# Kernel tuning notes

Hardware: AMD Instinct MI355X
Metric: run time of the kernel (lower is better)

Reference implementation:

```python
import jax, jax.numpy as jnp
import numpy as np


def setup_inputs() -> dict:
    key = jax.random.key(0)
    k1, k2, k3 = jax.random.split(key, 3)
    B, C, N, K, O = 8, 64, 4096, 16, 64
    x = jax.random.normal(k1, (B, C, N, 1), dtype=jnp.float32)
    # 1x1 Conv2d weights (out, in*2), biases (out)
    W_edge = jax.random.normal(k2, (O, 2 * C), dtype=jnp.float32) * 0.05
    b_edge = jnp.zeros((O,), dtype=jnp.float32)
    W_att = jax.random.normal(k3, (O, 2 * C), dtype=jnp.float32) * 0.05
    b_att = jnp.zeros((O,), dtype=jnp.float32)
    return {"x": x, "W_edge": W_edge, "b_edge": b_edge,
            "W_att": W_att, "b_att": b_att, "k": K}


def reference(x, W_edge, b_edge, W_att, b_att, k):
    # x: (B, C, N, 1)
    xt = jnp.transpose(x[..., 0], (0, 2, 1))  # (B, N, C)

    # --- dense KNN via pairwise squared distance (no-grad in original) ---
    xd = jax.lax.stop_gradient(xt)
    sq = jnp.sum(xd * xd, axis=-1, keepdims=True)           # (B, N, 1)
    dist = sq - 2.0 * jnp.einsum('bnc,bmc->bnm', xd, xd) + jnp.transpose(sq, (0, 2, 1))
    _, nn_idx = jax.lax.top_k(-dist, k)                      # (B, N, k)

    # --- gather neighbor features ---
    x_j = jax.vmap(lambda feat, idx: feat[idx])(xt, nn_idx)  # (B, N, k, C)
    # center index gather is identity: x_i[b,n,kk] = xt[b,n]
    x_i = jnp.broadcast_to(xt[:, :, None, :], x_j.shape)     # (B, N, k, C)

    feat = jnp.concatenate([x_i, x_j - x_i], axis=-1)        # (B, N, k, 2C)

    # 1x1 convs == per-point linear over channels
    edge = jnp.einsum('bnkc,oc->bnko', feat, W_edge) + b_edge  # (B, N, k, O)
    attn = jnp.einsum('bnkc,oc->bnko', feat, W_att) + b_att
    attn = jax.nn.softmax(attn, axis=2)                        # softmax over k

    out = jnp.sum(edge * attn, axis=2)                         # (B, N, O)
    # match torch output layout (B, O, N, 1)
    return jnp.transpose(out, (0, 2, 1))[..., None]
```

## Files before the change

### kernel.cpp

```cpp
#include <hip/hip_runtime.h>
#include <hip/hip_bf16.h>
#include <stdint.h>

#define NB 8
#define NC 64
#define NN 4096
#define NK 16
#define NO 64
#define TILE 64
#define NCHUNK 2
#define CHCOLS (NN / NCHUNK)
#define NTILES (CHCOLS / TILE)
#define NKL 16
#define NKC 32
#define PQS 160

typedef __attribute__((ext_vector_type(8))) short bf16x8;
typedef __attribute__((ext_vector_type(4))) float f32x4;

__device__ __forceinline__ unsigned umin32(unsigned a, unsigned b) { return a < b ? a : b; }
__device__ __forceinline__ unsigned shflx(unsigned v, int m) {
  return (unsigned)__shfl_xor((int)v, m);
}
__device__ __forceinline__ unsigned fmap(float x) {
  unsigned u = __float_as_uint(x);
  return u ^ ((unsigned)((int)u >> 31) | 0x80000000u);
}

__device__ __forceinline__ void cvt16bf(const float4 st[4], uint4& lo, uint4& hi) {
  union { float4 v[4]; float f[16]; } in;
  in.v[0] = st[0]; in.v[1] = st[1]; in.v[2] = st[2]; in.v[3] = st[3];
  union { unsigned short h[16]; uint4 v[2]; } out;
  #pragma unroll
  for (int i = 0; i < 16; ++i) {
    __hip_bfloat16 hh = __float2bfloat16(in.f[i]);
    out.h[i] = *reinterpret_cast<unsigned short*>(&hh);
  }
  lo = out.v[0]; hi = out.v[1];
}

__global__ __launch_bounds__(256) void proj_kernel(
    const float* __restrict__ x, const float* __restrict__ We,
    const float* __restrict__ be, const float* __restrict__ Wa,
    float* __restrict__ PQ, float* __restrict__ sq,
    float* __restrict__ XT)
{
  __shared__ float xs[NC][TILE];
  __shared__ float wt[NC][192];
  const int bid = blockIdx.x;
  const int b   = bid >> 6;
  const int n0  = (bid & 63) * TILE;
  const int tid = threadIdx.x;

  const float4* xg4 = (const float4*)x;
  float4* xs4 = (float4*)xs;
  for (int i = tid; i < NC * TILE / 4; i += 256) {
    int c = i >> 4, p4 = i & 15;
    xs4[c * 16 + p4] = xg4[(b * NC + c) * (NN / 4) + (n0 >> 2) + p4];
  }
  for (int i = tid; i < 64 * NC; i += 256) {
    int o = i >> 6, c = i & 63;
    float w1 = We[o * 128 + c], w2 = We[o * 128 + 64 + c];
    wt[c][o]        = w1 - w2;
    wt[c][64 + o]   = w2;
    wt[c][128 + o]  = Wa[o * 128 + 64 + c];
  }
  __syncthreads();

  {
    const int p = tid & 63, cg = tid >> 6;
    float4 v4[4];
    #pragma unroll
    for (int g = 0; g < 4; ++g) {
      v4[g].x = xs[cg * 16 + g * 4 + 0][p];
      v4[g].y = xs[cg * 16 + g * 4 + 1][p];
      v4[g].z = xs[cg * 16 + g * 4 + 2][p];
      v4[g].w = xs[cg * 16 + g * 4 + 3][p];
    }
    float4* Xp = (float4*)(XT + ((size_t)(b * NN + n0 + p) * NC + cg * 16));
    Xp[0] = v4[0]; Xp[1] = v4[1]; Xp[2] = v4[2]; Xp[3] = v4[3];
  }

  if (tid >= 192) {
    int p = tid - 192;
    float s = 0.f;
    #pragma unroll
    for (int c = 0; c < NC; ++c) { float v = xs[c][p]; s = fmaf(v, v, s); }
    sq[b * NN + n0 + p] = s;
  } else {
    const int r = tid;
    float wreg[NC];
    #pragma unroll
    for (int c = 0; c < NC; ++c) wreg[c] = wt[c][r];
    const float bias = (r < 64) ? be[r] : 0.f;
    for (int p = 0; p < TILE; p += 4) {
      float a0 = bias, a1 = bias, a2 = bias, a3 = bias;
      #pragma unroll
      for (int c = 0; c < NC; ++c) {
        float4 xv = *(const float4*)&xs[c][p];
        a0 = fmaf(wreg[c], xv.x, a0);
        a1 = fmaf(wreg[c], xv.y, a1);
        a2 = fmaf(wreg[c], xv.z, a2);
        a3 = fmaf(wreg[c], xv.w, a3);
      }
      if (r < 128) {
        size_t base = (size_t)(b * NN + n0 + p) * PQS + r;
        PQ[base]           = a0;
        PQ[base + PQS]     = a1;
        PQ[base + 2 * PQS] = a2;
        PQ[base + 3 * PQS] = a3;
      } else {
        const int o = r - 128;
        unsigned short* qb = (unsigned short*)((char*)PQ + (size_t)(b * NN + n0 + p) * (PQS * 4) + 512) + o;
        const size_t stride = PQS * 2;
        __hip_bfloat16 h0 = __float2bfloat16(a0);
        __hip_bfloat16 h1 = __float2bfloat16(a1);
        __hip_bfloat16 h2 = __float2bfloat16(a2);
        __hip_bfloat16 h3 = __float2bfloat16(a3);
        qb[0]          = *reinterpret_cast<unsigned short*>(&h0);
        qb[stride]     = *reinterpret_cast<unsigned short*>(&h1);
        qb[2 * stride] = *reinterpret_cast<unsigned short*>(&h2);
        qb[3 * stride] = *reinterpret_cast<unsigned short*>(&h3);
      }
    }
  }
}

__global__ __launch_bounds__(256) void knn_kernel(
    const float* __restrict__ XT, const float* __restrict__ sq,
    unsigned short* __restrict__ cand)
{
  __shared__ unsigned short Hc[2][64 * 64];
  __shared__ unsigned short Hr[64 * 64];

  const int bid = blockIdx.x;
  const int b   = bid >> 7;
  const int rt  = (bid >> 1) & 63;
  const int ch  = bid & 1;
  const int r0  = rt * TILE;
  const int c0  = ch * CHCOLS;
  const int tid = threadIdx.x;
  const int w    = tid >> 6;
  const int lane = tid & 63;
  const int lm   = lane & 15;
  const int lk   = lane >> 4;

  const float* Xb  = XT + (size_t)b * NN * NC;
  const float* sqg = sq + (size_t)b * NN;

  const int rowS = tid >> 2, subS = tid & 3;
  const int bytS = rowS * 128 + subS * 32;
  const int swzS = (rowS & 7) << 4;

  {
    float4 st[4]; uint4 lo, hi;
    const float4* srcR = (const float4*)(Xb + (size_t)(r0 + rowS) * NC + subS * 16);
    st[0]=srcR[0]; st[1]=srcR[1]; st[2]=srcR[2]; st[3]=srcR[3];
    cvt16bf(st, lo, hi);
    *(uint4*)((char*)Hr + ((bytS)      ^ swzS)) = lo;
    *(uint4*)((char*)Hr + ((bytS + 16) ^ swzS)) = hi;
    const float4* srcC = (const float4*)(Xb + (size_t)(c0 + rowS) * NC + subS * 16);
    st[0]=srcC[0]; st[1]=srcC[1]; st[2]=srcC[2]; st[3]=srcC[3];
    cvt16bf(st, lo, hi);
    *(uint4*)((char*)Hc[0] + ((bytS)      ^ swzS)) = lo;
    *(uint4*)((char*)Hc[0] + ((bytS + 16) ^ swzS)) = hi;
  }
  __syncthreads();

  const int brow = w * 16 + lm;
  const int bswz = (brow & 7) << 4;
  const bf16x8 bf0 = *(const bf16x8*)((const char*)Hr + ((brow * 128 + lk * 16)      ^ bswz));
  const bf16x8 bf1 = *(const bf16x8*)((const char*)Hr + ((brow * 128 + lk * 16 + 64) ^ bswz));

  unsigned bv[NKL];
  #pragma unroll
  for (int t = 0; t < NKL; ++t) bv[t] = 0xFFFFFFFFu;
  unsigned rowGuard = 0xFFFFFFFFu;

  for (int t = 0; t < NTILES; ++t) {
    const int cur = t & 1;
    float4 st[4];
    const bool doStage = (t + 1 < NTILES);
    if (doStage) {
      const float4* src = (const float4*)(Xb + (size_t)(c0 + (t + 1) * TILE + rowS) * NC + subS * 16);
      st[0]=src[0]; st[1]=src[1]; st[2]=src[2]; st[3]=src[3];
    }
    const int n1 = c0 + t * TILE;

    f32x4 acc[4];
    #pragma unroll
    for (int ct = 0; ct < 4; ++ct) acc[ct] = (f32x4){0.f, 0.f, 0.f, 0.f};
    #pragma unroll
    for (int ct = 0; ct < 4; ++ct) {
      const int arow = ct * 16 + lm;
      const int aswz = (arow & 7) << 4;
      bf16x8 a0 = *(const bf16x8*)((const char*)Hc[cur] + ((arow * 128 + lk * 16)      ^ aswz));
      bf16x8 a1 = *(const bf16x8*)((const char*)Hc[cur] + ((arow * 128 + lk * 16 + 64) ^ aswz));
      acc[ct] = __builtin_amdgcn_mfma_f32_16x16x32_bf16(a0, bf0, acc[ct], 0, 0, 0);
      acc[ct] = __builtin_amdgcn_mfma_f32_16x16x32_bf16(a1, bf1, acc[ct], 0, 0, 0);
    }

    unsigned d[16];
    #pragma unroll
    for (int ct = 0; ct < 4; ++ct) {
      const float4 s4 = *(const float4*)&sqg[n1 + ct * 16 + lk * 4];
      const int cbase = (t << 6) + (ct << 4) + (lk << 2);
      d[ct*4+0] = (fmap(fmaf(-2.f, acc[ct][0], s4.x)) & 0xFFFFF800u) | (unsigned)(cbase + 0);
      d[ct*4+1] = (fmap(fmaf(-2.f, acc[ct][1], s4.y)) & 0xFFFFF800u) | (unsigned)(cbase + 1);
      d[ct*4+2] = (fmap(fmaf(-2.f, acc[ct][2], s4.z)) & 0xFFFFF800u) | (unsigned)(cbase + 2);
      d[ct*4+3] = (fmap(fmaf(-2.f, acc[ct][3], s4.w)) & 0xFFFFF800u) | (unsigned)(cbase + 3);
    }

    unsigned m = d[0];
    #pragma unroll
    for (int i = 1; i < 16; ++i) m = umin32(m, d[i]);
    unsigned guard = umin32(bv[NKL - 1], rowGuard);
    #pragma unroll 1
    for (int rnd = 0; rnd < 16; ++rnd) {
      bool ins = m < guard;
      if (!__any(ins)) break;
      unsigned x  = ins ? m : 0xFFFFFFFFu;
      const unsigned xv = x;
      #pragma unroll
      for (int i = 0; i < NKL; ++i) {
        unsigned lo = umin32(bv[i], x);
        x = bv[i] < x ? x : bv[i];
        bv[i] = lo;
      }
      #pragma unroll
      for (int i = 0; i < 16; ++i) d[i] = (d[i] == xv) ? 0xFFFFFFFFu : d[i];
      m = d[0];
      #pragma unroll
      for (int i = 1; i < 16; ++i) m = umin32(m, d[i]);
      unsigned g15 = bv[NKL - 1];
      g15 = umin32(g15, shflx(g15, 16));
      g15 = umin32(g15, shflx(g15, 32));
      rowGuard = g15;
      guard = rowGuard;
    }

    if (doStage) {
      uint4 lo, hi;
      cvt16bf(st, lo, hi);
      *(uint4*)((char*)Hc[cur ^ 1] + ((bytS)      ^ swzS)) = lo;
      *(uint4*)((char*)Hc[cur ^ 1] + ((bytS + 16) ^ swzS)) = hi;
    }
    __syncthreads();
  }

  unsigned* mv = (unsigned*)&Hc[0][0];
  const int myrow = w * 16 + lm;
  __syncthreads();
  #pragma unroll
  for (int t = 0; t < NKL; ++t) mv[(myrow * 4 + lk) * NKL + t] = bv[t];
  __syncthreads();
  if (lk == 0) {
    for (int s2 = 1; s2 < 4; ++s2) {
      for (int t = 0; t < NKL; ++t) {
        unsigned v = mv[(myrow * 4 + s2) * NKL + t];
        if (v >= bv[NKL - 1]) break;
        unsigned x = v;
        #pragma unroll
        for (int q = 0; q < NKL; ++q) {
          unsigned lo = umin32(bv[q], x);
          x = bv[q] < x ? x : bv[q];
          bv[q] = lo;
        }
      }
    }
    unsigned short* cp = cand + (size_t)(b * NN + r0 + myrow) * NKC + ch * NKL;
    #pragma unroll
    for (int t = 0; t < NKL; ++t)
      cp[t] = (unsigned short)((bv[t] & 0x7FFu) + c0);
  }
}

__global__ __launch_bounds__(256) void rescore_kernel(
    const float* __restrict__ XT, const float* __restrict__ sq,
    unsigned short* __restrict__ cand, int* __restrict__ nn_idx)
{
  __shared__ float dv[8][NKC];
  __shared__ unsigned short di[8][NKC];
  const int tid  = threadIdx.x;
  const int w    = tid >> 6;
  const int lane = tid & 63;
  const int rowL = w * 2 + (lane >> 5);
  const int q    = lane & 31;
  const int row  = blockIdx.x * 8 + rowL;
  const int b = row >> 12, n = row & (NN - 1);
  const float* xt  = XT + (size_t)b * NN * NC;
  const float* sqg = sq + (size_t)b * NN;

  const int j = (int)cand[(size_t)row * NKC + q];
  const float4* cj = (const float4*)(xt + (size_t)j * NC);
  const float4* cn = (const float4*)(xt + (size_t)n * NC);
  float s = 0.f;
  #pragma unroll
  for (int i = 0; i < 16; ++i) {
    float4 a = cn[i], bb = cj[i];
    s = fmaf(a.x, bb.x, s);
    s = fmaf(a.y, bb.y, s);
    s = fmaf(a.z, bb.z, s);
    s = fmaf(a.w, bb.w, s);
  }
  dv[rowL][q] = fmaf(-2.f, s, sqg[j]);
  di[rowL][q] = (unsigned short)j;
  __syncthreads();

  if (tid < 8) {
    const int row2 = blockIdx.x * 8 + tid;
    float bvv[NK]; int bbi[NK];
    #pragma unroll
    for (int p = 0; p < NK; ++p) { bvv[p] = 3.0e38f; bbi[p] = 0; }
    for (int t = 0; t < NKC; ++t) {
      float v = dv[tid][t];
      if (v < bvv[NK - 1]) {
        bvv[NK - 1] = v; bbi[NK - 1] = (int)di[tid][t];
        #pragma unroll
        for (int p = NK - 1; p > 0; --p) {
          if (bvv[p] < bvv[p - 1]) {
            float tv = bvv[p]; bvv[p] = bvv[p - 1]; bvv[p - 1] = tv;
            int   ti = bbi[p]; bbi[p] = bbi[p - 1]; bbi[p - 1] = ti;
          }
        }
      }
    }
    int* np = nn_idx + (size_t)row2 * NK;
    #pragma unroll
    for (int p = 0; p < NK; ++p) np[p] = bbi[p];
  }
}

__global__ __launch_bounds__(256) void out_kernel(
    const float* __restrict__ PQ, const int* __restrict__ nn_idx,
    float* __restrict__ out)
{
  __shared__ float ot[TILE][TILE + 1];
  const int bid = blockIdx.x;
  const int b   = bid >> 6;
  const int n0  = (bid & 63) * TILE;
  const int tid = threadIdx.x;
  const int w = tid >> 6, o = tid & 63;

  for (int pi = 0; pi < 16; ++pi) {
    const int p = w * 16 + pi;
    const int n = n0 + p;
    const float* pqn = PQ + (size_t)(b * NN + n) * PQS;
    const float p1b  = pqn[o];
    const int* idxp  = nn_idx + (size_t)(b * NN + n) * NK;
    float p2[NK], q2[NK];
    #pragma unroll
    for (int t = 0; t < NK; ++t) {
      int jn = idxp[t];
      const float* pqj = PQ + (size_t)(b * NN + jn) * PQS;
      p2[t] = pqj[64 + o];
      unsigned short qh = ((const unsigned short*)(pqj + 128))[o];
      q2[t] = __bfloat162float(*reinterpret_cast<__hip_bfloat16*>(&qh));
    }
    float m = q2[0];
    #pragma unroll
    for (int t = 1; t < NK; ++t) m = fmaxf(m, q2[t]);
    float s = 0.f, num = 0.f;
    #pragma unroll
    for (int t = 0; t < NK; ++t) {
      float e = __expf(q2[t] - m);
      s += e;
      num = fmaf(e, p1b + p2[t], num);
    }
    ot[p][o] = num / s;
  }
  __syncthreads();

  const int oo = tid >> 2, qq = tid & 3;
  float* og = out + (size_t)(b * NO + oo) * NN + n0 + qq * 16;
  #pragma unroll
  for (int i = 0; i < 4; ++i) {
    float4 v;
    v.x = ot[qq * 16 + i * 4 + 0][oo];
    v.y = ot[qq * 16 + i * 4 + 1][oo];
    v.z = ot[qq * 16 + i * 4 + 2][oo];
    v.w = ot[qq * 16 + i * 4 + 3][oo];
    *(float4*)&og[i * 4] = v;
  }
}

extern "C" void kernel_launch(void* const* d_in, const int* in_sizes, int n_in,
                              void* d_out, int out_size, void* d_ws, size_t ws_size,
                              hipStream_t stream)
{
  const float* x  = (const float*)d_in[0];
  const float* We = (const float*)d_in[1];
  const float* be = (const float*)d_in[2];
  const float* Wa = (const float*)d_in[3];
  float* out = (float*)d_out;

  char* ws = (char*)d_ws;
  size_t off = 0;
  float* sq = (float*)(ws + off);                  off += (size_t)NB * NN * 4;
  float* PQ = (float*)(ws + off);                  off += (size_t)NB * NN * PQS * 4;
  float* XT = (float*)(ws + off);                  off += (size_t)NB * NN * NC * 4;
  unsigned short* cand = (unsigned short*)(ws + off);
  int* nn = (int*)cand;

  dim3 blk(256);
  proj_kernel<<<dim3(NB * (NN / TILE)), blk, 0, stream>>>(x, We, be, Wa, PQ, sq, XT);
  knn_kernel<<<dim3(NB * (NN / TILE) * NCHUNK), blk, 0, stream>>>(XT, sq, cand);
  rescore_kernel<<<dim3(NB * NN / 8), blk, 0, stream>>>(XT, sq, cand, nn);
  out_kernel<<<dim3(NB * (NN / TILE)), blk, 0, stream>>>(PQ, nn, out);
}
```

Measured before the change: 292.9 us.

## Precompute bf16 features, store projections in bf16, add fast-reject in KNN

The projection kernel now writes a bf16 copy of the transposed features, so the KNN kernel streams half the bytes and no longer converts from fp32 on every tile load. The P1/P2 projection table is stored in bf16 (192 shorts per point) instead of mixed fp32/bf16, which halves the gather traffic in the output kernel. The KNN inner loop first takes a float minimum and skips building packed keys when no lane can beat its current guard. The cost is lower precision in the P projections and an extra bf16 buffer written by proj_kernel.

Result: faster. 284.2 us (-3.0%).

```diff
diff --git a/kernel.cpp b/kernel.cpp
--- a/kernel.cpp
+++ b/kernel.cpp
@@ -13,7 +13,6 @@
 #define NTILES (CHCOLS / TILE)
 #define NKL 16
 #define NKC 32
-#define PQS 160
 
 typedef __attribute__((ext_vector_type(8))) short bf16x8;
 typedef __attribute__((ext_vector_type(4))) float f32x4;
@@ -26,24 +25,19 @@
   unsigned u = __float_as_uint(x);
   return u ^ ((unsigned)((int)u >> 31) | 0x80000000u);
 }
-
-__device__ __forceinline__ void cvt16bf(const float4 st[4], uint4& lo, uint4& hi) {
-  union { float4 v[4]; float f[16]; } in;
-  in.v[0] = st[0]; in.v[1] = st[1]; in.v[2] = st[2]; in.v[3] = st[3];
-  union { unsigned short h[16]; uint4 v[2]; } out;
-  #pragma unroll
-  for (int i = 0; i < 16; ++i) {
-    __hip_bfloat16 hh = __float2bfloat16(in.f[i]);
-    out.h[i] = *reinterpret_cast<unsigned short*>(&hh);
-  }
-  lo = out.v[0]; hi = out.v[1];
+__device__ __forceinline__ float bf2f(unsigned short h) {
+  return __bfloat162float(*reinterpret_cast<__hip_bfloat16*>(&h));
+}
+__device__ __forceinline__ unsigned short f2bfu(float v) {
+  __hip_bfloat16 hh = __float2bfloat16(v);
+  return *reinterpret_cast<unsigned short*>(&hh);
 }
 
 __global__ __launch_bounds__(256) void proj_kernel(
     const float* __restrict__ x, const float* __restrict__ We,
     const float* __restrict__ be, const float* __restrict__ Wa,
-    float* __restrict__ PQ, float* __restrict__ sq,
-    float* __restrict__ XT)
+    unsigned short* __restrict__ PQb, float* __restrict__ sq,
+    float* __restrict__ XT, unsigned short* __restrict__ H)
 {
   __shared__ float xs[NC][TILE];
   __shared__ float wt[NC][192];
@@ -69,16 +63,21 @@
 
   {
     const int p = tid & 63, cg = tid >> 6;
-    float4 v4[4];
+    union { float4 v4[4]; float f[16]; } vv;
     #pragma unroll
     for (int g = 0; g < 4; ++g) {
-      v4[g].x = xs[cg * 16 + g * 4 + 0][p];
-      v4[g].y = xs[cg * 16 + g * 4 + 1][p];
-      v4[g].z = xs[cg * 16 + g * 4 + 2][p];
-      v4[g].w = xs[cg * 16 + g * 4 + 3][p];
+      vv.v4[g].x = xs[cg * 16 + g * 4 + 0][p];
+      vv.v4[g].y = xs[cg * 16 + g * 4 + 1][p];
+      vv.v4[g].z = xs[cg * 16 + g * 4 + 2][p];
+      vv.v4[g].w = xs[cg * 16 + g * 4 + 3][p];
     }
     float4* Xp = (float4*)(XT + ((size_t)(b * NN + n0 + p) * NC + cg * 16));
-    Xp[0] = v4[0]; Xp[1] = v4[1]; Xp[2] = v4[2]; Xp[3] = v4[3];
+    Xp[0] = vv.v4[0]; Xp[1] = vv.v4[1]; Xp[2] = vv.v4[2]; Xp[3] = vv.v4[3];
+    union { unsigned short h[16]; uint4 u[2]; } hs;
+    #pragma unroll
+    for (int i = 0; i < 16; ++i) hs.h[i] = f2bfu(vv.f[i]);
+    uint4* Hp = (uint4*)(H + ((size_t)(b * NN + n0 + p) * NC + cg * 16));
+    Hp[0] = hs.u[0]; Hp[1] = hs.u[1];
   }
 
   if (tid >= 192) {
@@ -103,31 +102,17 @@
         a2 = fmaf(wreg[c], xv.z, a2);
         a3 = fmaf(wreg[c], xv.w, a3);
       }
-      if (r < 128) {
-        size_t base = (size_t)(b * NN + n0 + p) * PQS + r;
-        PQ[base]           = a0;
-        PQ[base + PQS]     = a1;
-        PQ[base + 2 * PQS] = a2;
-        PQ[base + 3 * PQS] = a3;
-      } else {
-        const int o = r - 128;
-        unsigned short* qb = (unsigned short*)((char*)PQ + (size_t)(b * NN + n0 + p) * (PQS * 4) + 512) + o;
-        const size_t stride = PQS * 2;
-        __hip_bfloat16 h0 = __float2bfloat16(a0);
-        __hip_bfloat16 h1 = __float2bfloat16(a1);
-        __hip_bfloat16 h2 = __float2bfloat16(a2);
-        __hip_bfloat16 h3 = __float2bfloat16(a3);
-        qb[0]          = *reinterpret_cast<unsigned short*>(&h0);
-        qb[stride]     = *reinterpret_cast<unsigned short*>(&h1);
-        qb[2 * stride] = *reinterpret_cast<unsigned short*>(&h2);
-        qb[3 * stride] = *reinterpret_cast<unsigned short*>(&h3);
-      }
+      size_t base = (size_t)(b * NN + n0 + p) * 192 + r;
+      PQb[base]           = f2bfu(a0);
+      PQb[base + 192]     = f2bfu(a1);
+      PQb[base + 2*192]   = f2bfu(a2);
+      PQb[base + 3*192]   = f2bfu(a3);
     }
   }
 }
 
 __global__ __launch_bounds__(256) void knn_kernel(
-    const float* __restrict__ XT, const float* __restrict__ sq,
+    const unsigned short* __restrict__ H, const float* __restrict__ sq,
     unsigned short* __restrict__ cand)
 {
   __shared__ unsigned short Hc[2][64 * 64];
@@ -145,7 +130,7 @@
   const int lm   = lane & 15;
   const int lk   = lane >> 4;
 
-  const float* Xb  = XT + (size_t)b * NN * NC;
+  const unsigned short* Hb = H + (size_t)b * NN * NC;
   const float* sqg = sq + (size_t)b * NN;
 
   const int rowS = tid >> 2, subS = tid & 3;
@@ -153,17 +138,12 @@
   const int swzS = (rowS & 7) << 4;
 
   {
-    float4 st[4]; uint4 lo, hi;
-    const float4* srcR = (const float4*)(Xb + (size_t)(r0 + rowS) * NC + subS * 16);
-    st[0]=srcR[0]; st[1]=srcR[1]; st[2]=srcR[2]; st[3]=srcR[3];
-    cvt16bf(st, lo, hi);
-    *(uint4*)((char*)Hr + ((bytS)      ^ swzS)) = lo;
-    *(uint4*)((char*)Hr + ((bytS + 16) ^ swzS)) = hi;
-    const float4* srcC = (const float4*)(Xb + (size_t)(c0 + rowS) * NC + subS * 16);
-    st[0]=srcC[0]; st[1]=srcC[1]; st[2]=srcC[2]; st[3]=srcC[3];
-    cvt16bf(st, lo, hi);
-    *(uint4*)((char*)Hc[0] + ((bytS)      ^ swzS)) = lo;
-    *(uint4*)((char*)Hc[0] + ((bytS + 16) ^ swzS)) = hi;
+    const uint4* srcR = (const uint4*)(Hb + (size_t)(r0 + rowS) * NC + subS * 16);
+    *(uint4*)((char*)Hr + ((bytS)      ^ swzS)) = srcR[0];
+    *(uint4*)((char*)Hr + ((bytS + 16) ^ swzS)) = srcR[1];
+    const uint4* srcC = (const uint4*)(Hb + (size_t)(c0 + rowS) * NC + subS * 16);
+    *(uint4*)((char*)Hc[0] + ((bytS)      ^ swzS)) = srcC[0];
+    *(uint4*)((char*)Hc[0] + ((bytS + 16) ^ swzS)) = srcC[1];
   }
   __syncthreads();
 
@@ -179,11 +159,11 @@
 
   for (int t = 0; t < NTILES; ++t) {
     const int cur = t & 1;
-    float4 st[4];
+    uint4 st0, st1;
     const bool doStage = (t + 1 < NTILES);
     if (doStage) {
-      const float4* src = (const float4*)(Xb + (size_t)(c0 + (t + 1) * TILE + rowS) * NC + subS * 16);
-      st[0]=src[0]; st[1]=src[1]; st[2]=src[2]; st[3]=src[3];
+      const uint4* src = (const uint4*)(Hb + (size_t)(c0 + (t + 1) * TILE + rowS) * NC + subS * 16);
+      st0 = src[0]; st1 = src[1];
     }
     const int n1 = c0 + t * TILE;
 
@@ -200,50 +180,63 @@
       acc[ct] = __builtin_amdgcn_mfma_f32_16x16x32_bf16(a1, bf1, acc[ct], 0, 0, 0);
     }
 
-    unsigned d[16];
+    float dd[16];
     #pragma unroll
     for (int ct = 0; ct < 4; ++ct) {
       const float4 s4 = *(const float4*)&sqg[n1 + ct * 16 + lk * 4];
-      const int cbase = (t << 6) + (ct << 4) + (lk << 2);
-      d[ct*4+0] = (fmap(fmaf(-2.f, acc[ct][0], s4.x)) & 0xFFFFF800u) | (unsigned)(cbase + 0);
-      d[ct*4+1] = (fmap(fmaf(-2.f, acc[ct][1], s4.y)) & 0xFFFFF800u) | (unsigned)(cbase + 1);
-      d[ct*4+2] = (fmap(fmaf(-2.f, acc[ct][2], s4.z)) & 0xFFFFF800u) | (unsigned)(cbase + 2);
-      d[ct*4+3] = (fmap(fmaf(-2.f, acc[ct][3], s4.w)) & 0xFFFFF800u) | (unsigned)(cbase + 3);
-    }
-
-    unsigned m = d[0];
-    #pragma unroll
-    for (int i = 1; i < 16; ++i) m = umin32(m, d[i]);
+      dd[ct*4+0] = fmaf(-2.f, acc[ct][0], s4.x);
+      dd[ct*4+1] = fmaf(-2.f, acc[ct][1], s4.y);
+      dd[ct*4+2] = fmaf(-2.f, acc[ct][2], s4.z);
+      dd[ct*4+3] = fmaf(-2.f, acc[ct][3], s4.w);
+    }
+    float fm = dd[0];
+    #pragma unroll
+    for (int i = 1; i < 16; ++i) fm = fminf(fm, dd[i]);
+
     unsigned guard = umin32(bv[NKL - 1], rowGuard);
-    #pragma unroll 1
-    for (int rnd = 0; rnd < 16; ++rnd) {
-      bool ins = m < guard;
-      if (!__any(ins)) break;
-      unsigned x  = ins ? m : 0xFFFFFFFFu;
-      const unsigned xv = x;
+    const unsigned t1 = fmap(fm) & 0xFFFFF800u;
+    if (__any(t1 < guard)) {
+      unsigned pd[16];
       #pragma unroll
-      for (int i = 0; i < NKL; ++i) {
-        unsigned lo = umin32(bv[i], x);
-        x = bv[i] < x ? x : bv[i];
-        bv[i] = lo;
+      for (int ct = 0; ct < 4; ++ct) {
+        const int cbase = (t << 6) + (ct << 4) + (lk << 2);
+        pd[ct*4+0] = (fmap(dd[ct*4+0]) & 0xFFFFF800u) | (unsigned)(cbase + 0);
+        pd[ct*4+1] = (fmap(dd[ct*4+1]) & 0xFFFFF800u) | (unsigned)(cbase + 1);
+        pd[ct*4+2] = (fmap(dd[ct*4+2]) & 0xFFFFF800u) | (unsigned)(cbase + 2);
+        pd[ct*4+3] = (fmap(dd[ct*4+3]) & 0xFFFFF800u) | (unsigned)(cbase + 3);
       }
+      unsigned pm = pd[0];
       #pragma unroll
-      for (int i = 0; i < 16; ++i) d[i] = (d[i] == xv) ? 0xFFFFFFFFu : d[i];
-      m = d[0];
-      #pragma unroll
-      for (int i = 1; i < 16; ++i) m = umin32(m, d[i]);
-      unsigned g15 = bv[NKL - 1];
-      g15 = umin32(g15, shflx(g15, 16));
-      g15 = umin32(g15, shflx(g15, 32));
-      rowGuard = g15;
-      guard = rowGuard;
+      for (int i = 1; i < 16; ++i) pm = umin32(pm, pd[i]);
+
+      #pragma unroll 1
+      for (int rnd = 0; rnd < 16; ++rnd) {
+        bool ins = pm < guard;
+        if (!__any(ins)) break;
+        unsigned x = ins ? pm : 0xFFFFFFFFu;
+        const unsigned xv = x;
+        #pragma unroll
+        for (int i = 0; i < NKL; ++i) {
+          unsigned lo = umin32(bv[i], x);
+          x = bv[i] < x ? x : bv[i];
+          bv[i] = lo;
+        }
+        #pragma unroll
+        for (int i = 0; i < 16; ++i) pd[i] = (pd[i] == xv) ? 0xFFFFFFFFu : pd[i];
+        pm = pd[0];
+        #pragma unroll
+        for (int i = 1; i < 16; ++i) pm = umin32(pm, pd[i]);
+        unsigned g15 = bv[NKL - 1];
+        g15 = umin32(g15, shflx(g15, 16));
+        g15 = umin32(g15, shflx(g15, 32));
+        rowGuard = g15;
+        guard = rowGuard;
+      }
     }
 
     if (doStage) {
-      uint4 lo, hi;
-      cvt16bf(st, lo, hi);
-      *(uint4*)((char*)Hc[cur ^ 1] + ((bytS)      ^ swzS)) = lo;
-      *(uint4*)((char*)Hc[cur ^ 1] + ((bytS + 16) ^ swzS)) = hi;
+      *(uint4*)((char*)Hc[cur ^ 1] + ((bytS)      ^ swzS)) = st0;
+      *(uint4*)((char*)Hc[cur ^ 1] + ((bytS + 16) ^ swzS)) = st1;
     }
     __syncthreads();
   }
@@ -332,7 +325,7 @@
 }
 
 __global__ __launch_bounds__(256) void out_kernel(
-    const float* __restrict__ PQ, const int* __restrict__ nn_idx,
+    const unsigned short* __restrict__ PQb, const int* __restrict__ nn_idx,
     float* __restrict__ out)
 {
   __shared__ float ot[TILE][TILE + 1];
@@ -345,17 +338,16 @@
   for (int pi = 0; pi < 16; ++pi) {
     const int p = w * 16 + pi;
     const int n = n0 + p;
-    const float* pqn = PQ + (size_t)(b * NN + n) * PQS;
-    const float p1b  = pqn[o];
+    const unsigned short* pqn = PQb + (size_t)(b * NN + n) * 192;
+    const float p1b  = bf2f(pqn[o]);
     const int* idxp  = nn_idx + (size_t)(b * NN + n) * NK;
     float p2[NK], q2[NK];
     #pragma unroll
     for (int t = 0; t < NK; ++t) {
       int jn = idxp[t];
-      const float* pqj = PQ + (size_t)(b * NN + jn) * PQS;
-      p2[t] = pqj[64 + o];
-      unsigned short qh = ((const unsigned short*)(pqj + 128))[o];
-      q2[t] = __bfloat162float(*reinterpret_cast<__hip_bfloat16*>(&qh));
+      const unsigned short* pqj = PQb + (size_t)(b * NN + jn) * 192;
+      p2[t] = bf2f(pqj[64 + o]);
+      q2[t] = bf2f(pqj[128 + o]);
     }
     float m = q2[0];
     #pragma unroll
@@ -396,15 +388,16 @@
 
   char* ws = (char*)d_ws;
   size_t off = 0;
-  float* sq = (float*)(ws + off);                  off += (size_t)NB * NN * 4;
-  float* PQ = (float*)(ws + off);                  off += (size_t)NB * NN * PQS * 4;
-  float* XT = (float*)(ws + off);                  off += (size_t)NB * NN * NC * 4;
+  float* sq = (float*)(ws + off);                   off += (size_t)NB * NN * 4;
+  unsigned short* PQb = (unsigned short*)(ws + off); off += (size_t)NB * NN * 192 * 2;
+  float* XT = (float*)(ws + off);                   off += (size_t)NB * NN * NC * 4;
+  unsigned short* H = (unsigned short*)(ws + off);  off += (size_t)NB * NN * NC * 2;
   unsigned short* cand = (unsigned short*)(ws + off);
   int* nn = (int*)cand;
 
   dim3 blk(256);
-  proj_kernel<<<dim3(NB * (NN / TILE)), blk, 0, stream>>>(x, We, be, Wa, PQ, sq, XT);
-  knn_kernel<<<dim3(NB * (NN / TILE) * NCHUNK), blk, 0, stream>>>(XT, sq, cand);
+  proj_kernel<<<dim3(NB * (NN / TILE)), blk, 0, stream>>>(x, We, be, Wa, PQb, sq, XT, H);
+  knn_kernel<<<dim3(NB * (NN / TILE) * NCHUNK), blk, 0, stream>>>(H, sq, cand);
   rescore_kernel<<<dim3(NB * NN / 8), blk, 0, stream>>>(XT, sq, cand, nn);
-  out_kernel<<<dim3(NB * (NN / TILE)), blk, 0, stream>>>(PQ, nn, out);
-}
+  out_kernel<<<dim3(NB * (NN / TILE)), blk, 0, stream>>>(PQb, nn, out);
+}
```
